# Optimization experiments

Hardware: AMD Instinct MI355X
Metric: run time of the kernel (lower is better)

Reference implementation:

```python
import jax, jax.numpy as jnp
import numpy as np
import jax.lax as lax

KERNEL = 7
STRIDE = 1
PAD = 3

def setup_inputs() -> dict:
    key = jax.random.key(0)
    kx, kw = jax.random.split(key)
    x = jax.random.normal(kx, (64, 512, 512), dtype=jnp.float32)
    weight = jax.random.normal(kw, (KERNEL, KERNEL), dtype=jnp.float32)
    return {"x": x, "weight": weight}

def reference(x, weight):
    # x: [B, H, W] single-channel; weight: [k, k]
    # Original computes cross-correlation (no kernel flip) with zero padding.
    lhs = x[:, None, :, :]                      # [B, 1, H, W]
    rhs = weight[None, None, :, :]              # [O=1, I=1, k, k]
    out = lax.conv_general_dilated(
        lhs, rhs,
        window_strides=(STRIDE, STRIDE),
        padding=[(PAD, PAD), (PAD, PAD)],
        dimension_numbers=("NCHW", "OIHW", "NCHW"),
    )
    return out[:, 0, :, :]                      # [B, H_out, W_out]
```

## Files before the change

### kernel.cpp

```cpp
#include <hip/hip_runtime.h>
#include <stdint.h>


#define IMG_W 512
#define IMG_H 512
#define NIMG  64
#define TW    256
#define TH    16
#define HALO  3
#define LDS_W 264
#define LDS_H (TH + 2*HALO)

__device__ __forceinline__ void gload_lds16(const float* src, float* dst_lds)
{
    __builtin_amdgcn_global_load_lds(
        (__attribute__((address_space(1))) void*)(uintptr_t)src,
        (__attribute__((address_space(3))) void*)(uintptr_t)dst_lds,
        16, 0, 0);
}

__global__ __launch_bounds__(256, 6) void conv7x7_kernel(
    const float* __restrict__ x,
    const float* __restrict__ wgt,
    float* __restrict__ out)
{
    __shared__ float tile[LDS_H * LDS_W];

    const int tid  = threadIdx.x;
    const int wave = tid >> 6;
    const int lane = tid & 63;
    const int bx   = blockIdx.x * TW;
    const int by   = blockIdx.y * TH;
    const int n    = blockIdx.z;

    const float* img = x + (size_t)n * (IMG_W * IMG_H);

    float w[49];
    #pragma unroll
    for (int i = 0; i < 49; ++i) w[i] = wgt[i];

    for (int r = wave; r < LDS_H; r += 4) {
        const int gy = by - HALO + r;
        float* dst = &tile[r * LDS_W + 4 + 4 * lane];
        if ((unsigned)gy < IMG_H) {
            gload_lds16(&img[(size_t)gy * IMG_W + bx + 4 * lane], dst);
        } else {
            *(float4*)dst = make_float4(0.f, 0.f, 0.f, 0.f);
        }
    }

    if (tid < 2 * LDS_H) {
        const int r    = tid >> 1;
        const int side = tid & 1;
        const int cb   = side ? (LDS_W - 4) : 0;
        const int gx   = side ? (bx + 256) : (bx - 4);
        const int gy   = by - HALO + r;
        float4 v = make_float4(0.f, 0.f, 0.f, 0.f);
        if (((unsigned)gy < IMG_H) && ((unsigned)gx < IMG_W))
            v = *(const float4*)&img[(size_t)gy * IMG_W + gx];
        *(float4*)&tile[r * LDS_W + cb] = v;
    }

    __syncthreads();

    const int lx = lane * 4;
    const int rbase = wave * 4;

    int d[6];
    #pragma unroll
    for (int t = 0; t < 6; ++t) {
        d[t] = t * 8;
        asm volatile("" : "+v"(d[t]));
    }

    const char* tb = (const char*)tile + (size_t)(rbase * LDS_W + lx) * 4;

    float acc[4][4] = {};

    #pragma unroll
    for (int r = 0; r < 10; ++r) {
        const char* rowb = tb + (size_t)r * (LDS_W * 4);
        float2 q[6];
        #pragma unroll
        for (int t = 0; t < 6; ++t)
            q[t] = *(const float2*)(rowb + d[t]);
        const float row[12] = {q[0].x, q[0].y, q[1].x, q[1].y,
                               q[2].x, q[2].y, q[3].x, q[3].y,
                               q[4].x, q[4].y, q[5].x, q[5].y};
        #pragma unroll
        for (int j = 0; j < 4; ++j) {
            const int ky = r - j;
            if (ky >= 0 && ky < 7) {
                #pragma unroll
                for (int kx = 0; kx < 7; ++kx) {
                    const float wv = w[ky * 7 + kx];
                    #pragma unroll
                    for (int cc = 0; cc < 4; ++cc)
                        acc[j][cc] = fmaf(row[1 + kx + cc], wv, acc[j][cc]);
                }
            }
        }
    }

    float* o = out + (size_t)n * (IMG_W * IMG_H);
    #pragma unroll
    for (int j = 0; j < 4; ++j) {
        float4 v = make_float4(acc[j][0], acc[j][1], acc[j][2], acc[j][3]);
        *(float4*)&o[(size_t)(by + rbase + j) * IMG_W + bx + lx] = v;
    }
}

extern "C" void kernel_launch(void* const* d_in, const int* in_sizes, int n_in,
                              void* d_out, int out_size, void* d_ws, size_t ws_size,
                              hipStream_t stream)
{
    const float* x   = (const float*)d_in[0];
    const float* wgt = (const float*)d_in[1];
    float* out       = (float*)d_out;

    dim3 grid(IMG_W / TW, IMG_H / TH, NIMG);
    conv7x7_kernel<<<grid, 256, 0, stream>>>(x, wgt, out);
}
```

Before: 117.6 us.

## Process four row tiles per block with double-buffered LDS prefetch

Each block now walks four consecutive 16-row tiles instead of one. It prefetches the next tile into a second LDS buffer with async global-to-LDS loads while computing the current tile. This amortizes the weight loads and block launch overhead, and is meant to overlap global memory latency with FMA work. The cost is double the LDS per block, lower declared occupancy (launch bounds 6 to 3), and four times fewer blocks.

```diff
diff --git a/kernel.cpp b/kernel.cpp
--- a/kernel.cpp
+++ b/kernel.cpp
@@ -7,9 +7,11 @@
 #define NIMG  64
 #define TW    256
 #define TH    16
+#define TILES_Y 4
 #define HALO  3
 #define LDS_W 264
 #define LDS_H (TH + 2*HALO)
+#define TILE_F (LDS_H * LDS_W)
 
 __device__ __forceinline__ void gload_lds16(const float* src, float* dst_lds)
 {
@@ -19,36 +21,18 @@
         16, 0, 0);
 }
 
-__global__ __launch_bounds__(256, 6) void conv7x7_kernel(
-    const float* __restrict__ x,
-    const float* __restrict__ wgt,
-    float* __restrict__ out)
+__device__ __forceinline__ void stage_tile(float* buf, const float* __restrict__ img,
+                                           int bx, int by, int wave, int lane, int tid)
 {
-    __shared__ float tile[LDS_H * LDS_W];
-
-    const int tid  = threadIdx.x;
-    const int wave = tid >> 6;
-    const int lane = tid & 63;
-    const int bx   = blockIdx.x * TW;
-    const int by   = blockIdx.y * TH;
-    const int n    = blockIdx.z;
-
-    const float* img = x + (size_t)n * (IMG_W * IMG_H);
-
-    float w[49];
-    #pragma unroll
-    for (int i = 0; i < 49; ++i) w[i] = wgt[i];
-
     for (int r = wave; r < LDS_H; r += 4) {
         const int gy = by - HALO + r;
-        float* dst = &tile[r * LDS_W + 4 + 4 * lane];
+        float* dst = &buf[r * LDS_W + 4 + 4 * lane];
         if ((unsigned)gy < IMG_H) {
             gload_lds16(&img[(size_t)gy * IMG_W + bx + 4 * lane], dst);
         } else {
             *(float4*)dst = make_float4(0.f, 0.f, 0.f, 0.f);
         }
     }
-
     if (tid < 2 * LDS_H) {
         const int r    = tid >> 1;
         const int side = tid & 1;
@@ -58,10 +42,30 @@
         float4 v = make_float4(0.f, 0.f, 0.f, 0.f);
         if (((unsigned)gy < IMG_H) && ((unsigned)gx < IMG_W))
             v = *(const float4*)&img[(size_t)gy * IMG_W + gx];
-        *(float4*)&tile[r * LDS_W + cb] = v;
+        *(float4*)&buf[r * LDS_W + cb] = v;
     }
+}
 
-    __syncthreads();
+__global__ __launch_bounds__(256, 3) void conv7x7_kernel(
+    const float* __restrict__ x,
+    const float* __restrict__ wgt,
+    float* __restrict__ out)
+{
+    __shared__ float tile[2 * TILE_F];
+
+    const int tid  = threadIdx.x;
+    const int wave = tid >> 6;
+    const int lane = tid & 63;
+    const int bx   = blockIdx.x * TW;
+    const int by0  = blockIdx.y * (TH * TILES_Y);
+    const int n    = blockIdx.z;
+
+    const float* img = x + (size_t)n * (IMG_W * IMG_H);
+    float* o = out + (size_t)n * (IMG_W * IMG_H);
+
+    float w[49];
+    #pragma unroll
+    for (int i = 0; i < 49; ++i) w[i] = wgt[i];
 
     const int lx = lane * 4;
     const int rbase = wave * 4;
@@ -73,40 +77,55 @@
         asm volatile("" : "+v"(d[t]));
     }
 
-    const char* tb = (const char*)tile + (size_t)(rbase * LDS_W + lx) * 4;
+    stage_tile(&tile[0], img, bx, by0, wave, lane, tid);
+    __syncthreads();
 
-    float acc[4][4] = {};
+    int cur = 0;
+    #pragma unroll
+    for (int t = 0; t < TILES_Y; ++t) {
+        if (t < TILES_Y - 1)
+            stage_tile(&tile[(cur ^ 1) * TILE_F], img, bx, by0 + (t + 1) * TH,
+                       wave, lane, tid);
 
-    #pragma unroll
-    for (int r = 0; r < 10; ++r) {
-        const char* rowb = tb + (size_t)r * (LDS_W * 4);
-        float2 q[6];
+        const int by = by0 + t * TH;
+        const char* tb = (const char*)&tile[cur * TILE_F]
+                       + (size_t)(rbase * LDS_W + lx) * 4;
+
+        float acc[4][4] = {};
+
         #pragma unroll
-        for (int t = 0; t < 6; ++t)
-            q[t] = *(const float2*)(rowb + d[t]);
-        const float row[12] = {q[0].x, q[0].y, q[1].x, q[1].y,
-                               q[2].x, q[2].y, q[3].x, q[3].y,
-                               q[4].x, q[4].y, q[5].x, q[5].y};
-        #pragma unroll
-        for (int j = 0; j < 4; ++j) {
-            const int ky = r - j;
-            if (ky >= 0 && ky < 7) {
-                #pragma unroll
-                for (int kx = 0; kx < 7; ++kx) {
-                    const float wv = w[ky * 7 + kx];
+        for (int r = 0; r < 10; ++r) {
+            const char* rowb = tb + (size_t)r * (LDS_W * 4);
+            float2 q[6];
+            #pragma unroll
+            for (int u = 0; u < 6; ++u)
+                q[u] = *(const float2*)(rowb + d[u]);
+            const float row[12] = {q[0].x, q[0].y, q[1].x, q[1].y,
+                                   q[2].x, q[2].y, q[3].x, q[3].y,
+                                   q[4].x, q[4].y, q[5].x, q[5].y};
+            #pragma unroll
+            for (int j = 0; j < 4; ++j) {
+                const int ky = r - j;
+                if (ky >= 0 && ky < 7) {
                     #pragma unroll
-                    for (int cc = 0; cc < 4; ++cc)
-                        acc[j][cc] = fmaf(row[1 + kx + cc], wv, acc[j][cc]);
+                    for (int kx = 0; kx < 7; ++kx) {
+                        const float wv = w[ky * 7 + kx];
+                        #pragma unroll
+                        for (int cc = 0; cc < 4; ++cc)
+                            acc[j][cc] = fmaf(row[1 + kx + cc], wv, acc[j][cc]);
+                    }
                 }
             }
         }
-    }
 
-    float* o = out + (size_t)n * (IMG_W * IMG_H);
-    #pragma unroll
-    for (int j = 0; j < 4; ++j) {
-        float4 v = make_float4(acc[j][0], acc[j][1], acc[j][2], acc[j][3]);
-        *(float4*)&o[(size_t)(by + rbase + j) * IMG_W + bx + lx] = v;
+        #pragma unroll
+        for (int j = 0; j < 4; ++j) {
+            float4 v = make_float4(acc[j][0], acc[j][1], acc[j][2], acc[j][3]);
+            *(float4*)&o[(size_t)(by + rbase + j) * IMG_W + bx + lx] = v;
+        }
+
+        __syncthreads();
+        cur ^= 1;
     }
 }
 
@@ -118,6 +137,6 @@
     const float* wgt = (const float*)d_in[1];
     float* out       = (float*)d_out;
 
-    dim3 grid(IMG_W / TW, IMG_H / TH, NIMG);
+    dim3 grid(IMG_W / TW, IMG_H / (TH * TILES_Y), NIMG);
     conv7x7_kernel<<<grid, 256, 0, stream>>>(x, wgt, out);
 }
```

Result: slower. 125.0 us (+6.2%).
